# Optimization experiments

Hardware: AMD Instinct MI355X
Metric: run time of the kernel (lower is better)

## Reference

```python
import jax, jax.numpy as jnp
import numpy as np

B, C_IN, H, W = 16, 128, 224, 224
C_OUT, KH, KW = 256, 3, 3
STRIDE = (2, 3)
PAD = 1


def setup_inputs() -> dict:
    key = jax.random.key(0)
    kx, kw, kb = jax.random.split(key, 3)
    x = jax.random.normal(kx, (B, C_IN, H, W), dtype=jnp.float32)
    weight = jax.random.normal(kw, (C_OUT, C_IN, KH, KW), dtype=jnp.float32)
    bias = jax.random.normal(kb, (C_OUT,), dtype=jnp.float32)
    return {"x": x, "weight": weight, "bias": bias}


def reference(x, weight, bias):
    # Faithful conv2d: zero-pad by 1 on each side, stride (2,3), kernel 3x3,
    # per-output-channel dot product + bias (same math as the quadruple-loop torch code).
    out = jax.lax.conv_general_dilated(
        x, weight,
        window_strides=STRIDE,
        padding=[(PAD, PAD), (PAD, PAD)],
        dimension_numbers=("NCHW", "OIHW", "NCHW"),
    )
    return out + bias[None, :, None, None]
```

## Files before the change

### kernel.cpp

```cpp
#include <hip/hip_runtime.h>
#include <cstdint>

constexpr int B_   = 16;
constexpr int CIN  = 128;
constexpr int H_   = 224;
constexpr int W_   = 224;
constexpr int COUT = 256;
constexpr int HOUT = 112;
constexpr int WOUT = 75;

constexpr int OWP   = 80;
constexpr int CI_SC = 16;
constexpr int KSC_R = 144;
constexpr int KP    = 160;
constexpr int NSC   = 8;
constexpr int THREADS = 256;

constexpr int WS_SH8  = COUT * KP * NSC / 8;
constexpr size_t WS_NEED = (size_t)WS_SH8 * 16;

constexpr int B_OFF   = 25600;
constexpr int LDS_TOT = B_OFF + 3 * 16384;

typedef float  f32x4   __attribute__((ext_vector_type(4)));
typedef short  short8  __attribute__((ext_vector_type(8)));
typedef unsigned int uint32x4 __attribute__((ext_vector_type(4)));

struct U64x2 { unsigned long long lo, hi; };
__device__ inline short8 bc8(unsigned long long a, unsigned long long b) {
  U64x2 u{a, b};
  return __builtin_bit_cast(short8, u);
}
__device__ inline short8 cv8(uint32x4 v) { return __builtin_bit_cast(short8, v); }

__device__ inline unsigned cvtpk(float a, float b) {
  unsigned r;
  asm("v_cvt_pk_bf16_f32 %0, %1, %2" : "=v"(r) : "v"(a), "v"(b));
  return r;
}

__device__ __forceinline__ void gload_lds(const void* g, void* l) {
  __builtin_amdgcn_global_load_lds((const __attribute__((address_space(1))) void*)g,
                                   (__attribute__((address_space(3))) void*)l, 16, 0, 0);
}

__global__ __launch_bounds__(256) void wprep(const float* __restrict__ wgt,
                                             uint4* __restrict__ ws) {
  int o  = blockIdx.x * 256 + threadIdx.x;
  int co = o & 255;
  int t  = o >> 8;
  int g  = t & 3;
  int u  = t >> 2;
  int kc = u % 5;
  int sc = u / 5;
  int kloc = kc * 32 + g * 8;
  float f[8];
  if (kloc < KSC_R) {
    const float* p = wgt + (size_t)co * 1152 + sc * KSC_R + kloc;
    float4 a = *(const float4*)p;
    float4 b = *(const float4*)(p + 4);
    f[0] = a.x; f[1] = a.y; f[2] = a.z; f[3] = a.w;
    f[4] = b.x; f[5] = b.y; f[6] = b.z; f[7] = b.w;
  } else {
#pragma unroll
    for (int e = 0; e < 8; ++e) f[e] = 0.f;
  }
  ws[o] = uint4{cvtpk(f[0], f[1]), cvtpk(f[2], f[3]), cvtpk(f[4], f[5]), cvtpk(f[6], f[7])};
}

__device__ __forceinline__ short8 load_bq(const float* q, int kc, int g) {
  if (kc == 4 && g >= 2) return short8{};
  const float* s = q + kc * 32;
  float4 x0 = *(const float4*)s, x1 = *(const float4*)(s + 4);
  uint4 u{cvtpk(x0.x, x0.y), cvtpk(x0.z, x0.w), cvtpk(x1.x, x1.y), cvtpk(x1.z, x1.w)};
  return __builtin_bit_cast(short8, u);
}

#define TR_ISSUE(S, KC)                                                                   \
  {                                                                                       \
    unsigned a_ = abase + (unsigned)((KC) * 5120);                                        \
    asm volatile("ds_read_b64_tr_b16 %0, %1"             : "=v"(S##0) : "v"(a_));         \
    asm volatile("ds_read_b64_tr_b16 %0, %1 offset:640"  : "=v"(S##1) : "v"(a_));         \
    asm volatile("ds_read_b64_tr_b16 %0, %1 offset:128"  : "=v"(S##2) : "v"(a_));         \
    asm volatile("ds_read_b64_tr_b16 %0, %1 offset:768"  : "=v"(S##3) : "v"(a_));         \
    asm volatile("ds_read_b64_tr_b16 %0, %1 offset:256"  : "=v"(S##4) : "v"(a_));         \
    asm volatile("ds_read_b64_tr_b16 %0, %1 offset:896"  : "=v"(S##5) : "v"(a_));         \
    asm volatile("ds_read_b64_tr_b16 %0, %1 offset:384"  : "=v"(S##6) : "v"(a_));         \
    asm volatile("ds_read_b64_tr_b16 %0, %1 offset:1024" : "=v"(S##7) : "v"(a_));         \
    asm volatile("ds_read_b64_tr_b16 %0, %1 offset:512"  : "=v"(S##8) : "v"(a_));         \
    asm volatile("ds_read_b64_tr_b16 %0, %1 offset:1152" : "=v"(S##9) : "v"(a_));         \
  }

#define B_ISSUE(BR, BB)                                                                   \
  asm volatile("ds_read_b128 %0, %1"             : "=v"(BR##0) : "v"(BB));                \
  asm volatile("ds_read_b128 %0, %1 offset:1024" : "=v"(BR##1) : "v"(BB));                \
  asm volatile("ds_read_b128 %0, %1 offset:2048" : "=v"(BR##2) : "v"(BB));                \
  asm volatile("ds_read_b128 %0, %1 offset:3072" : "=v"(BR##3) : "v"(BB));

#define B_DMA(GT, BS)                                                                     \
  {                                                                                       \
    const char* s_ = wsl + (size_t)(GT) * 16384;                                          \
    char* d_ = bD + (BS) * 16384;                                                         \
    gload_lds(s_,       d_);                                                              \
    gload_lds(s_ + 256, d_ + 1024);                                                       \
    gload_lds(s_ + 512, d_ + 2048);                                                       \
    gload_lds(s_ + 768, d_ + 3072);                                                       \
  }

#define VMGATE(N)                                                                         \
  asm volatile("s_waitcnt vmcnt(" #N ")" ::: "memory");                                   \
  __builtin_amdgcn_sched_barrier(0);

#define WAITLG(N)                                                                         \
  asm volatile("s_waitcnt lgkmcnt(" #N ")" ::: "memory");                                 \
  __builtin_amdgcn_sched_barrier(0);

#define MFMA_SET(S, B0, B1, B2, B3)                                                       \
  {                                                                                       \
    short8 a0_ = bc8(S##0, S##1);                                                         \
    short8 a1_ = bc8(S##2, S##3);                                                         \
    short8 a2_ = bc8(S##4, S##5);                                                         \
    short8 a3_ = bc8(S##6, S##7);                                                         \
    short8 a4_ = bc8(S##8, S##9);                                                         \
    __builtin_amdgcn_s_setprio(1);                                                        \
    acc[0][0] = __builtin_amdgcn_mfma_f32_16x16x32_bf16(a0_, B0, acc[0][0], 0, 0, 0);     \
    acc[0][1] = __builtin_amdgcn_mfma_f32_16x16x32_bf16(a0_, B1, acc[0][1], 0, 0, 0);     \
    acc[0][2] = __builtin_amdgcn_mfma_f32_16x16x32_bf16(a0_, B2, acc[0][2], 0, 0, 0);     \
    acc[0][3] = __builtin_amdgcn_mfma_f32_16x16x32_bf16(a0_, B3, acc[0][3], 0, 0, 0);     \
    acc[1][0] = __builtin_amdgcn_mfma_f32_16x16x32_bf16(a1_, B0, acc[1][0], 0, 0, 0);     \
    acc[1][1] = __builtin_amdgcn_mfma_f32_16x16x32_bf16(a1_, B1, acc[1][1], 0, 0, 0);     \
    acc[1][2] = __builtin_amdgcn_mfma_f32_16x16x32_bf16(a1_, B2, acc[1][2], 0, 0, 0);     \
    acc[1][3] = __builtin_amdgcn_mfma_f32_16x16x32_bf16(a1_, B3, acc[1][3], 0, 0, 0);     \
    acc[2][0] = __builtin_amdgcn_mfma_f32_16x16x32_bf16(a2_, B0, acc[2][0], 0, 0, 0);     \
    acc[2][1] = __builtin_amdgcn_mfma_f32_16x16x32_bf16(a2_, B1, acc[2][1], 0, 0, 0);     \
    acc[2][2] = __builtin_amdgcn_mfma_f32_16x16x32_bf16(a2_, B2, acc[2][2], 0, 0, 0);     \
    acc[2][3] = __builtin_amdgcn_mfma_f32_16x16x32_bf16(a2_, B3, acc[2][3], 0, 0, 0);     \
    acc[3][0] = __builtin_amdgcn_mfma_f32_16x16x32_bf16(a3_, B0, acc[3][0], 0, 0, 0);     \
    acc[3][1] = __builtin_amdgcn_mfma_f32_16x16x32_bf16(a3_, B1, acc[3][1], 0, 0, 0);     \
    acc[3][2] = __builtin_amdgcn_mfma_f32_16x16x32_bf16(a3_, B2, acc[3][2], 0, 0, 0);     \
    acc[3][3] = __builtin_amdgcn_mfma_f32_16x16x32_bf16(a3_, B3, acc[3][3], 0, 0, 0);     \
    acc[4][0] = __builtin_amdgcn_mfma_f32_16x16x32_bf16(a4_, B0, acc[4][0], 0, 0, 0);     \
    acc[4][1] = __builtin_amdgcn_mfma_f32_16x16x32_bf16(a4_, B1, acc[4][1], 0, 0, 0);     \
    acc[4][2] = __builtin_amdgcn_mfma_f32_16x16x32_bf16(a4_, B2, acc[4][2], 0, 0, 0);     \
    acc[4][3] = __builtin_amdgcn_mfma_f32_16x16x32_bf16(a4_, B3, acc[4][3], 0, 0, 0);     \
    __builtin_amdgcn_s_setprio(0);                                                        \
  }

template <int WS>
__global__ __launch_bounds__(THREADS, 2) void conv_mfma(
    const float* __restrict__ x, const float* __restrict__ wgt,
    const short8* __restrict__ wbf, const float* __restrict__ bias,
    float* __restrict__ out) {

  __shared__ __align__(16) unsigned char smem[LDS_TOT];

  int Lid = (blockIdx.x & 7) * 224 + (blockIdx.x >> 3);
  int oh  = Lid % 112;
  int b   = Lid / 112;

  const int tid   = threadIdx.x;
  const int lane  = tid & 63;
  const int cogrp = tid >> 6;
  const int g     = lane >> 4;
  const int l15   = lane & 15;

  const float* xb = x + (size_t)b * CIN * H_ * W_;
  const int coB_  = cogrp * 64 + l15;

  const unsigned sbase = (unsigned)(uintptr_t)&smem[0];
  const unsigned abase = sbase + (unsigned)(g * 1280 + l15 * 8);
  const unsigned vB    = sbase + (unsigned)(B_OFF + cogrp * 4096 + lane * 16);
  char* bD = (char*)&smem[B_OFF + cogrp * 4096];
  const char* wsl = (const char*)wbf + (size_t)(g * 4096 + cogrp * 1024 + l15 * 16);

  if (tid < 160) {
    *reinterpret_cast<uint4*>(&smem[23040 + tid * 16]) = uint4{0u, 0u, 0u, 0u};
  }

  f32x4 acc[5][4];
#pragma unroll
  for (int mf = 0; mf < 5; ++mf)
#pragma unroll
    for (int cf = 0; cf < 4; ++cf)
#pragma unroll
      for (int i = 0; i < 4; ++i) acc[mf][cf][i] = 0.f;

  unsigned long long tA0, tA1, tA2, tA3, tA4, tA5, tA6, tA7, tA8, tA9;
  unsigned long long tB0, tB1, tB2, tB3, tB4, tB5, tB6, tB7, tB8, tB9;
  uint32x4 brA0, brA1, brA2, brA3, brB0, brB1, brB2, brB3;

  int bsel = 0, gkc = 0, gt;
  unsigned bb;
  if (WS) { B_DMA(0, 0) B_DMA(1, 1) B_DMA(2, 2) }

  for (int sc = 0; sc < NSC; ++sc) {
    if (sc) __syncthreads();

    const float* xs = xb + (size_t)sc * (CI_SC * H_ * W_);
#pragma unroll
    for (int j = 0; j < 4; ++j) {
      int it = tid + THREADS * j;
      if (j < 3 || it < 912) {
        int gg  = it % 19;
        int rid = it / 19;
        int ci  = rid & 15;
        int kh  = rid >> 4;
        int ih  = 2 * oh - 1 + kh;
        bool rowok = (unsigned)ih < (unsigned)H_;
        int ro  = (ci * H_ + (rowok ? ih : 0)) * W_;
        int iwb = 12 * gg;
        unsigned mAj = rowok ? 0xFFFFFFFFu : 0u;
        unsigned mFj = mAj & (gg ? 0xFFFFFFFFu : 0xFFFF0000u);

        const float* ap = xs + (ro + iwb);
        float4 a4 = *(const float4*)ap;
        float4 b4 = *(const float4*)(ap + 4);
        float4 c4 = *(const float4*)(xs + (ro + (iwb + 8 > 220 ? 220 : iwb + 8)));
        float fm1 = xs[ro + iwb - (gg ? 1 : 0)];

        int k = ci * 9 + kh * 3;
        int m = 4 * gg;
        unsigned base = (unsigned)(((k >> 2) * 5 + (m >> 4)) * 128 + (m & 15) * 2);
        unsigned o0 = base + (unsigned)((k & 3) * 32);
        unsigned o1 = base + (unsigned)(((k + 1) & 3) * 32) + (((k + 1) >> 2) - (k >> 2)) * 640u;
        unsigned o2 = base + (unsigned)(((k + 2) & 3) * 32) + (((k + 2) >> 2) - (k >> 2)) * 640u;

        unsigned l0 = cvtpk(fm1,  a4.z) & mFj;
        unsigned h0 = cvtpk(b4.y, c4.x) & mAj;
        unsigned l1 = cvtpk(a4.x, a4.w) & mAj;
        unsigned h1 = cvtpk(b4.z, c4.y) & mAj;
        unsigned l2 = cvtpk(a4.y, b4.x) & mAj;
        unsigned h2 = cvtpk(b4.w, c4.z) & mAj;
        *(uint2*)&smem[o0] = make_uint2(l0, h0);
        *(uint2*)&smem[o1] = make_uint2(l1, h1);
        *(uint2*)&smem[o2] = make_uint2(l2, h2);
      }
    }
    __syncthreads();

    if (WS) {
      const int b1 = bsel + 1 == 3 ? 0 : bsel + 1;
      const int b2 = b1 + 1 == 3 ? 0 : b1 + 1;

      VMGATE(8);
      bb = vB + (unsigned)bsel * 16384u;
      B_ISSUE(brA, bb);
      TR_ISSUE(tA, 0);

      VMGATE(4);
      bb = vB + (unsigned)b1 * 16384u;
      B_ISSUE(brB, bb);
      TR_ISSUE(tB, 1);
      WAITLG(14);
      { short8 c0 = cv8(brA0), c1 = cv8(brA1), c2 = cv8(brA2), c3 = cv8(brA3);
        MFMA_SET(tA, c0, c1, c2, c3); }
      gt = gkc + 3; if (gt > 39) gt = 39;
      B_DMA(gt, bsel);
      ++gkc;

      VMGATE(4);
      bb = vB + (unsigned)b2 * 16384u;
      B_ISSUE(brA, bb);
      TR_ISSUE(tA, 2);
      WAITLG(14);
      { short8 c0 = cv8(brB0), c1 = cv8(brB1), c2 = cv8(brB2), c3 = cv8(brB3);
        MFMA_SET(tB, c0, c1, c2, c3); }
      gt = gkc + 3; if (gt > 39) gt = 39;
      B_DMA(gt, b1);
      ++gkc;

      VMGATE(4);
      bb = vB + (unsigned)bsel * 16384u;
      B_ISSUE(brB, bb);
      TR_ISSUE(tB, 3);
      WAITLG(14);
      { short8 c0 = cv8(brA0), c1 = cv8(brA1), c2 = cv8(brA2), c3 = cv8(brA3);
        MFMA_SET(tA, c0, c1, c2, c3); }
      gt = gkc + 3; if (gt > 39) gt = 39;
      B_DMA(gt, b2);
      ++gkc;

      VMGATE(4);
      bb = vB + (unsigned)b1 * 16384u;
      B_ISSUE(brA, bb);
      TR_ISSUE(tA, 4);
      WAITLG(14);
      { short8 c0 = cv8(brB0), c1 = cv8(brB1), c2 = cv8(brB2), c3 = cv8(brB3);
        MFMA_SET(tB, c0, c1, c2, c3); }
      gt = gkc + 3; if (gt > 39) gt = 39;
      B_DMA(gt, bsel);
      ++gkc;

      WAITLG(0);
      { short8 c0 = cv8(brA0), c1 = cv8(brA1), c2 = cv8(brA2), c3 = cv8(brA3);
        MFMA_SET(tA, c0, c1, c2, c3); }
      gt = gkc + 3; if (gt > 39) gt = 39;
      B_DMA(gt, b1);
      ++gkc;

      bsel = b2;
    } else {
      const float* q0 = wgt + (size_t)coB_ * 1152 + sc * 144 + g * 8;
      const float* q1 = q0 + (size_t)16 * 1152;
      const float* q2 = q0 + (size_t)32 * 1152;
      const float* q3 = q0 + (size_t)48 * 1152;
#pragma unroll
      for (int kc = 0; kc < 5; ++kc) {
        short8 c0 = load_bq(q0, kc, g), c1 = load_bq(q1, kc, g);
        short8 c2 = load_bq(q2, kc, g), c3 = load_bq(q3, kc, g);
        TR_ISSUE(tA, kc);
        WAITLG(0);
        MFMA_SET(tA, c0, c1, c2, c3);
      }
    }
  }

  asm volatile("s_waitcnt vmcnt(0)" ::: "memory");

  float bv0 = bias[coB_];
  float bv1 = bias[coB_ + 16];
  float bv2 = bias[coB_ + 32];
  float bv3 = bias[coB_ + 48];
  size_t ob0 = (((size_t)b * COUT + coB_) * HOUT + oh) * WOUT;
  size_t ob1 = ob0 + (size_t)16 * HOUT * WOUT;
  size_t ob2 = ob0 + (size_t)32 * HOUT * WOUT;
  size_t ob3 = ob0 + (size_t)48 * HOUT * WOUT;
#pragma unroll
  for (int mf = 0; mf < 5; ++mf) {
    int owb = mf * 16 + g * 4;
#pragma unroll
    for (int r = 0; r < 4; ++r) {
      int ow = owb + r;
      if (ow < WOUT) {
        out[ob0 + ow] = acc[mf][0][r] + bv0;
        out[ob1 + ow] = acc[mf][1][r] + bv1;
        out[ob2 + ow] = acc[mf][2][r] + bv2;
        out[ob3 + ow] = acc[mf][3][r] + bv3;
      }
    }
  }
}

extern "C" void kernel_launch(void* const* d_in, const int* in_sizes, int n_in,
                              void* d_out, int out_size, void* d_ws, size_t ws_size,
                              hipStream_t stream) {
  const float* x    = (const float*)d_in[0];
  const float* wgt  = (const float*)d_in[1];
  const float* bias = (const float*)d_in[2];
  float* out        = (float*)d_out;

  dim3 grid(16 * 112);
  dim3 block(THREADS);

  if (ws_size >= WS_NEED) {
    wprep<<<dim3(WS_SH8 / 256), dim3(256), 0, stream>>>(wgt, (uint4*)d_ws);
    conv_mfma<1><<<grid, block, 0, stream>>>(x, wgt, (const short8*)d_ws, bias, out);
  } else {
    conv_mfma<0><<<grid, block, 0, stream>>>(x, wgt, (const short8*)d_ws, bias, out);
  }
}
```

Before: 200.3 us.

## Load weights directly to registers and prefetch next input stage during MFMAs

Drops the triple-buffered LDS DMA path for prepared bf16 weights and instead loads the weight fragments straight from global memory into registers, rotating three register sets across the five k-chunks. The first three rows of the next input-channel slice are prefetched into registers while the current slice's MFMAs run, overlapping global load latency with compute. This shrinks LDS usage, which may raise occupancy, but adds register pressure and puts global-load latency on the MFMA critical path. The lgkmcnt waits now also cover scalar or global loads, so the ordering of waits matters.

```diff
diff --git a/kernel.cpp b/kernel.cpp
--- a/kernel.cpp
+++ b/kernel.cpp
@@ -9,7 +9,6 @@
 constexpr int HOUT = 112;
 constexpr int WOUT = 75;
 
-constexpr int OWP   = 80;
 constexpr int CI_SC = 16;
 constexpr int KSC_R = 144;
 constexpr int KP    = 160;
@@ -19,29 +18,19 @@
 constexpr int WS_SH8  = COUT * KP * NSC / 8;
 constexpr size_t WS_NEED = (size_t)WS_SH8 * 16;
 
-constexpr int B_OFF   = 25600;
-constexpr int LDS_TOT = B_OFF + 3 * 16384;
-
 typedef float  f32x4   __attribute__((ext_vector_type(4)));
 typedef short  short8  __attribute__((ext_vector_type(8)));
-typedef unsigned int uint32x4 __attribute__((ext_vector_type(4)));
 
 struct U64x2 { unsigned long long lo, hi; };
 __device__ inline short8 bc8(unsigned long long a, unsigned long long b) {
   U64x2 u{a, b};
   return __builtin_bit_cast(short8, u);
 }
-__device__ inline short8 cv8(uint32x4 v) { return __builtin_bit_cast(short8, v); }
 
 __device__ inline unsigned cvtpk(float a, float b) {
   unsigned r;
   asm("v_cvt_pk_bf16_f32 %0, %1, %2" : "=v"(r) : "v"(a), "v"(b));
   return r;
-}
-
-__device__ __forceinline__ void gload_lds(const void* g, void* l) {
-  __builtin_amdgcn_global_load_lds((const __attribute__((address_space(1))) void*)g,
-                                   (__attribute__((address_space(3))) void*)l, 16, 0, 0);
 }
 
 __global__ __launch_bounds__(256) void wprep(const float* __restrict__ wgt,
@@ -91,25 +80,11 @@
     asm volatile("ds_read_b64_tr_b16 %0, %1 offset:1152" : "=v"(S##9) : "v"(a_));         \
   }
 
-#define B_ISSUE(BR, BB)                                                                   \
-  asm volatile("ds_read_b128 %0, %1"             : "=v"(BR##0) : "v"(BB));                \
-  asm volatile("ds_read_b128 %0, %1 offset:1024" : "=v"(BR##1) : "v"(BB));                \
-  asm volatile("ds_read_b128 %0, %1 offset:2048" : "=v"(BR##2) : "v"(BB));                \
-  asm volatile("ds_read_b128 %0, %1 offset:3072" : "=v"(BR##3) : "v"(BB));
-
-#define B_DMA(GT, BS)                                                                     \
-  {                                                                                       \
-    const char* s_ = wsl + (size_t)(GT) * 16384;                                          \
-    char* d_ = bD + (BS) * 16384;                                                         \
-    gload_lds(s_,       d_);                                                              \
-    gload_lds(s_ + 256, d_ + 1024);                                                       \
-    gload_lds(s_ + 512, d_ + 2048);                                                       \
-    gload_lds(s_ + 768, d_ + 3072);                                                       \
-  }
-
-#define VMGATE(N)                                                                         \
-  asm volatile("s_waitcnt vmcnt(" #N ")" ::: "memory");                                   \
-  __builtin_amdgcn_sched_barrier(0);
+#define BLOADR(X, KC)                                                                     \
+  X##0 = wsb[(KC) * 1024];                                                                \
+  X##1 = wsb[(KC) * 1024 + 16];                                                           \
+  X##2 = wsb[(KC) * 1024 + 32];                                                           \
+  X##3 = wsb[(KC) * 1024 + 48];
 
 #define WAITLG(N)                                                                         \
   asm volatile("s_waitcnt lgkmcnt(" #N ")" ::: "memory");                                 \
@@ -146,13 +121,35 @@
     __builtin_amdgcn_s_setprio(0);                                                        \
   }
 
+#define STAGE_LOAD(SC)                                                                    \
+  {                                                                                       \
+    const float* xs_ = xb + (size_t)((SC) & 7) * (CI_SC * H_ * W_);                       \
+    _Pragma("unroll")                                                                     \
+    for (int j = 0; j < 3; ++j) {                                                         \
+      int it  = tid + THREADS * j;                                                        \
+      int gg  = it % 19;                                                                  \
+      int rid = it / 19;                                                                  \
+      int ci  = rid & 15;                                                                 \
+      int kh  = rid >> 4;                                                                 \
+      int ih  = 2 * oh - 1 + kh;                                                          \
+      bool rowok = (unsigned)ih < (unsigned)H_;                                           \
+      int ro  = (ci * H_ + (rowok ? ih : 0)) * W_;                                        \
+      int iwb = 12 * gg;                                                                  \
+      const float* ap = xs_ + (ro + iwb);                                                 \
+      pa[j] = *(const float4*)ap;                                                         \
+      pb[j] = *(const float4*)(ap + 4);                                                   \
+      pc[j] = *(const float4*)(xs_ + (ro + (iwb + 8 > 220 ? 220 : iwb + 8)));             \
+      pm[j] = xs_[ro + iwb - (gg ? 1 : 0)];                                               \
+    }                                                                                     \
+  }
+
 template <int WS>
 __global__ __launch_bounds__(THREADS, 2) void conv_mfma(
     const float* __restrict__ x, const float* __restrict__ wgt,
     const short8* __restrict__ wbf, const float* __restrict__ bias,
     float* __restrict__ out) {
 
-  __shared__ __align__(16) unsigned char smem[LDS_TOT];
+  __shared__ __align__(16) unsigned char smem[KP * 80 * 2];
 
   int Lid = (blockIdx.x & 7) * 224 + (blockIdx.x >> 3);
   int oh  = Lid % 112;
@@ -169,9 +166,6 @@
 
   const unsigned sbase = (unsigned)(uintptr_t)&smem[0];
   const unsigned abase = sbase + (unsigned)(g * 1280 + l15 * 8);
-  const unsigned vB    = sbase + (unsigned)(B_OFF + cogrp * 4096 + lane * 16);
-  char* bD = (char*)&smem[B_OFF + cogrp * 4096];
-  const char* wsl = (const char*)wbf + (size_t)(g * 4096 + cogrp * 1024 + l15 * 16);
 
   if (tid < 160) {
     *reinterpret_cast<uint4*>(&smem[23040 + tid * 16]) = uint4{0u, 0u, 0u, 0u};
@@ -187,13 +181,17 @@
 
   unsigned long long tA0, tA1, tA2, tA3, tA4, tA5, tA6, tA7, tA8, tA9;
   unsigned long long tB0, tB1, tB2, tB3, tB4, tB5, tB6, tB7, tB8, tB9;
-  uint32x4 brA0, brA1, brA2, brA3, brB0, brB1, brB2, brB3;
-
-  int bsel = 0, gkc = 0, gt;
-  unsigned bb;
-  if (WS) { B_DMA(0, 0) B_DMA(1, 1) B_DMA(2, 2) }
+  short8 bX0, bX1, bX2, bX3, bY0, bY1, bY2, bY3, bZ0, bZ1, bZ2, bZ3;
+  float4 pa[3], pb[3], pc[3];
+  float  pm[3];
+
+  STAGE_LOAD(0);
 
   for (int sc = 0; sc < NSC; ++sc) {
+    const short8* wsb = wbf + (size_t)sc * 5120 + g * 256 + cogrp * 64 + l15;
+
+    if (WS) { BLOADR(bX, 0) BLOADR(bY, 1) }
+
     if (sc) __syncthreads();
 
     const float* xs = xb + (size_t)sc * (CI_SC * H_ * W_);
@@ -207,16 +205,22 @@
         int kh  = rid >> 4;
         int ih  = 2 * oh - 1 + kh;
         bool rowok = (unsigned)ih < (unsigned)H_;
-        int ro  = (ci * H_ + (rowok ? ih : 0)) * W_;
-        int iwb = 12 * gg;
         unsigned mAj = rowok ? 0xFFFFFFFFu : 0u;
         unsigned mFj = mAj & (gg ? 0xFFFFFFFFu : 0xFFFF0000u);
 
-        const float* ap = xs + (ro + iwb);
-        float4 a4 = *(const float4*)ap;
-        float4 b4 = *(const float4*)(ap + 4);
-        float4 c4 = *(const float4*)(xs + (ro + (iwb + 8 > 220 ? 220 : iwb + 8)));
-        float fm1 = xs[ro + iwb - (gg ? 1 : 0)];
+        float4 a4, b4, c4;
+        float fm1;
+        if (j < 3) {
+          a4 = pa[j]; b4 = pb[j]; c4 = pc[j]; fm1 = pm[j];
+        } else {
+          int ro  = (ci * H_ + (rowok ? ih : 0)) * W_;
+          int iwb = 12 * gg;
+          const float* ap = xs + (ro + iwb);
+          a4 = *(const float4*)ap;
+          b4 = *(const float4*)(ap + 4);
+          c4 = *(const float4*)(xs + (ro + (iwb + 8 > 220 ? 220 : iwb + 8)));
+          fm1 = xs[ro + iwb - (gg ? 1 : 0)];
+        }
 
         int k = ci * 9 + kh * 3;
         int m = 4 * gg;
@@ -239,71 +243,31 @@
     __syncthreads();
 
     if (WS) {
-      const int b1 = bsel + 1 == 3 ? 0 : bsel + 1;
-      const int b2 = b1 + 1 == 3 ? 0 : b1 + 1;
-
-      VMGATE(8);
-      bb = vB + (unsigned)bsel * 16384u;
-      B_ISSUE(brA, bb);
       TR_ISSUE(tA, 0);
-
-      VMGATE(4);
-      bb = vB + (unsigned)b1 * 16384u;
-      B_ISSUE(brB, bb);
       TR_ISSUE(tB, 1);
-      WAITLG(14);
-      { short8 c0 = cv8(brA0), c1 = cv8(brA1), c2 = cv8(brA2), c3 = cv8(brA3);
-        MFMA_SET(tA, c0, c1, c2, c3); }
-      gt = gkc + 3; if (gt > 39) gt = 39;
-      B_DMA(gt, bsel);
-      ++gkc;
-
-      VMGATE(4);
-      bb = vB + (unsigned)b2 * 16384u;
-      B_ISSUE(brA, bb);
+      BLOADR(bZ, 2)
+      WAITLG(10);
+      MFMA_SET(tA, bX0, bX1, bX2, bX3);
       TR_ISSUE(tA, 2);
-      WAITLG(14);
-      { short8 c0 = cv8(brB0), c1 = cv8(brB1), c2 = cv8(brB2), c3 = cv8(brB3);
-        MFMA_SET(tB, c0, c1, c2, c3); }
-      gt = gkc + 3; if (gt > 39) gt = 39;
-      B_DMA(gt, b1);
-      ++gkc;
-
-      VMGATE(4);
-      bb = vB + (unsigned)bsel * 16384u;
-      B_ISSUE(brB, bb);
+      BLOADR(bX, 3)
+      WAITLG(10);
+      MFMA_SET(tB, bY0, bY1, bY2, bY3);
+      STAGE_LOAD(sc + 1);
       TR_ISSUE(tB, 3);
-      WAITLG(14);
-      { short8 c0 = cv8(brA0), c1 = cv8(brA1), c2 = cv8(brA2), c3 = cv8(brA3);
-        MFMA_SET(tA, c0, c1, c2, c3); }
-      gt = gkc + 3; if (gt > 39) gt = 39;
-      B_DMA(gt, b2);
-      ++gkc;
-
-      VMGATE(4);
-      bb = vB + (unsigned)b1 * 16384u;
-      B_ISSUE(brA, bb);
+      BLOADR(bY, 4)
+      WAITLG(10);
+      MFMA_SET(tA, bZ0, bZ1, bZ2, bZ3);
       TR_ISSUE(tA, 4);
-      WAITLG(14);
-      { short8 c0 = cv8(brB0), c1 = cv8(brB1), c2 = cv8(brB2), c3 = cv8(brB3);
-        MFMA_SET(tB, c0, c1, c2, c3); }
-      gt = gkc + 3; if (gt > 39) gt = 39;
-      B_DMA(gt, bsel);
-      ++gkc;
-
+      WAITLG(10);
+      MFMA_SET(tB, bX0, bX1, bX2, bX3);
       WAITLG(0);
-      { short8 c0 = cv8(brA0), c1 = cv8(brA1), c2 = cv8(brA2), c3 = cv8(brA3);
-        MFMA_SET(tA, c0, c1, c2, c3); }
-      gt = gkc + 3; if (gt > 39) gt = 39;
-      B_DMA(gt, b1);
-      ++gkc;
-
-      bsel = b2;
+      MFMA_SET(tA, bY0, bY1, bY2, bY3);
     } else {
       const float* q0 = wgt + (size_t)coB_ * 1152 + sc * 144 + g * 8;
       const float* q1 = q0 + (size_t)16 * 1152;
       const float* q2 = q0 + (size_t)32 * 1152;
       const float* q3 = q0 + (size_t)48 * 1152;
+      STAGE_LOAD(sc + 1);
 #pragma unroll
       for (int kc = 0; kc < 5; ++kc) {
         short8 c0 = load_bq(q0, kc, g), c1 = load_bq(q1, kc, g);
@@ -314,8 +278,6 @@
       }
     }
   }
-
-  asm volatile("s_waitcnt vmcnt(0)" ::: "memory");
 
   float bv0 = bias[coB_];
   float bv1 = bias[coB_ + 16];
```

After: 222.9 us. 11.3% more time.
